# Performance work log

Measured on AMD Instinct MI355X. Metric: run time of the kernel, lower is better.

## Reference

```python
import jax, jax.numpy as jnp
import numpy as np

N_NODES = 524288
N_EDGES = 2097152
N_GRAPHS = 16384
COMP_DIM = 3539
PROT_DIM = 384
GNN_HID = 64
G_EMB = 128
HID = 256


def setup_inputs() -> dict:
    key = jax.random.key(0)
    ks = jax.random.split(key, 16)
    def lin(k, fan_in, fan_out):
        b = 1.0 / np.sqrt(fan_in)
        kw, kb = jax.random.split(k)
        return (jax.random.uniform(kw, (fan_in, fan_out), jnp.float32, -b, b),
                jax.random.uniform(kb, (fan_out,), jnp.float32, -b, b))
    W1, b1 = lin(ks[0], 1, GNN_HID)
    W2, b2 = lin(ks[1], GNN_HID, GNN_HID)
    Wg, bg = lin(ks[2], GNN_HID, G_EMB)
    Wf1, bf1 = lin(ks[3], G_EMB + COMP_DIM + PROT_DIM, HID)
    Wf2, bf2 = lin(ks[4], HID, 1)
    node_x = jax.random.normal(ks[5], (N_NODES, 1), jnp.float32)
    compound_feat = jax.random.normal(ks[6], (N_GRAPHS, COMP_DIM), jnp.float32)
    protein_feat = jax.random.normal(ks[7], (N_GRAPHS, PROT_DIM), jnp.float32)
    edge_index = jax.random.randint(ks[8], (2, N_EDGES), 0, N_NODES, jnp.int64 if jax.config.jax_enable_x64 else jnp.int32)
    batch = jnp.sort(jax.random.randint(ks[9], (N_NODES,), 0, N_GRAPHS, jnp.int32))
    return {"node_x": node_x, "compound_feat": compound_feat, "protein_feat": protein_feat,
            "edge_index": edge_index, "batch": batch,
            "W1": W1, "b1": b1, "W2": W2, "b2": b2, "Wg": Wg, "bg": bg,
            "Wf1": Wf1, "bf1": bf1, "Wf2": Wf2, "bf2": bf2}


def _gcn_norm(edge_index, num_nodes):
    # add self-loops, then symmetric normalization (PyG GCNConv default)
    loop = jnp.arange(num_nodes, dtype=edge_index.dtype)
    row = jnp.concatenate([edge_index[0], loop])
    col = jnp.concatenate([edge_index[1], loop])
    deg = jax.ops.segment_sum(jnp.ones_like(col, jnp.float32), col, num_segments=num_nodes)
    dinv = jnp.where(deg > 0, jax.lax.rsqrt(deg), 0.0)
    norm = dinv[row] * dinv[col]
    return row, col, norm


def _gcn_conv(x, W, b, row, col, norm, num_nodes):
    h = x @ W  # [N, out]
    out = jax.ops.segment_sum(norm[:, None] * h[row], col, num_segments=num_nodes)
    return out + b


def reference(node_x, compound_feat, protein_feat, edge_index, batch,
              W1, b1, W2, b2, Wg, bg, Wf1, bf1, Wf2, bf2):
    N = node_x.shape[0]
    B = compound_feat.shape[0]
    row, col, norm = _gcn_norm(edge_index, N)
    x = jax.nn.relu(_gcn_conv(node_x, W1, b1, row, col, norm, N))
    x = jax.nn.relu(_gcn_conv(x, W2, b2, row, col, norm, N))
    # global mean pool per graph
    sums = jax.ops.segment_sum(x, batch, num_segments=B)
    cnts = jax.ops.segment_sum(jnp.ones((N,), jnp.float32), batch, num_segments=B)
    pooled = sums / jnp.maximum(cnts, 1.0)[:, None]
    g = pooled @ Wg + bg  # [B, G_EMB]
    combined = jnp.concatenate([g, compound_feat, protein_feat], axis=1)
    h = jax.nn.relu(combined @ Wf1 + bf1)
    return jax.nn.sigmoid(h @ Wf2 + bf2)
```

## Files before the change

### kernel.cpp

```cpp
#include <hip/hip_runtime.h>

#define NN 524288
#define NE 2097152
#define NG 16384
#define CDIM 3539
#define PDIM 384
#define GH 64
#define GE 128
#define HIDD 256
#define KD (GE + CDIM + PDIM)
#define KP 4096

typedef short bf16x8 __attribute__((ext_vector_type(8)));
typedef unsigned short u16x8 __attribute__((ext_vector_type(8)));
typedef float f32x4 __attribute__((ext_vector_type(4)));

__device__ inline unsigned short f2bf(float f) {
    unsigned int u = __float_as_uint(f);
    u += 0x7FFF + ((u >> 16) & 1);
    return (unsigned short)(u >> 16);
}

__global__ void k_init(int* __restrict__ idg, float* __restrict__ sums) {
    int i = blockIdx.x * blockDim.x + threadIdx.x;
    if (i < NN) idg[i] = 0;
    if (i < NG * GH) sums[i] = 0.0f;
}

__global__ void k_deg(const int* __restrict__ ei, int* __restrict__ idg,
                      int* __restrict__ eseq) {
    int e = blockIdx.x * blockDim.x + threadIdx.x;
    eseq[e] = atomicAdd(&idg[ei[NE + e]], 1);
}

__global__ void k_prep(const float* __restrict__ node_x, const int* __restrict__ idg,
                       float2* __restrict__ f2a, int* __restrict__ ecnt) {
    int n = blockIdx.x * blockDim.x + threadIdx.x;
    int c = idg[n];
    float di = rsqrtf((float)(c + 1));
    f2a[n] = make_float2(di * node_x[n], di);
    ecnt[n] = c;
}

__global__ void k_cnt(const int* __restrict__ batch, float* __restrict__ cnt) {
    int g = blockIdx.x * 256 + threadIdx.x;
    int lo = 0, hi = NN;
    while (lo < hi) { int mid = (lo + hi) >> 1; if (batch[mid] < g) lo = mid + 1; else hi = mid; }
    int lo2 = lo, hi2 = NN;
    while (lo2 < hi2) { int mid = (lo2 + hi2) >> 1; if (batch[mid] < g + 1) lo2 = mid + 1; else hi2 = mid; }
    cnt[g] = (float)(lo2 - lo);
}

__global__ void k_scan1(const int* __restrict__ ecnt, int* __restrict__ bsum) {
    __shared__ int ls[256];
    int t = threadIdx.x;
    ls[t] = ecnt[blockIdx.x * 256 + t];
    __syncthreads();
    for (int d = 128; d > 0; d >>= 1) { if (t < d) ls[t] += ls[t + d]; __syncthreads(); }
    if (t == 0) bsum[blockIdx.x] = ls[0];
}

__global__ void k_scan2(int* __restrict__ bsum) {
    __shared__ int ls[256];
    int t = threadIdx.x;
    int loc[8]; int s = 0;
#pragma unroll
    for (int i = 0; i < 8; i++) { loc[i] = bsum[t * 8 + i]; s += loc[i]; }
    ls[t] = s; __syncthreads();
    for (int d = 1; d < 256; d <<= 1) {
        int add = (t >= d) ? ls[t - d] : 0; __syncthreads();
        ls[t] += add; __syncthreads();
    }
    int run = ls[t] - s;
#pragma unroll
    for (int i = 0; i < 8; i++) { int tmp = loc[i]; bsum[t * 8 + i] = run; run += tmp; }
}

__global__ void k_scan3(const int* __restrict__ ecnt, const int* __restrict__ bsum,
                        int* __restrict__ offs) {
    __shared__ int ls[256];
    int t = threadIdx.x, n = blockIdx.x * 256 + t;
    int v = ecnt[n];
    ls[t] = v; __syncthreads();
    for (int d = 1; d < 256; d <<= 1) {
        int add = (t >= d) ? ls[t - d] : 0; __syncthreads();
        ls[t] += add; __syncthreads();
    }
    offs[n] = bsum[blockIdx.x] + ls[t] - v;
    if (n == 0) offs[NN] = NE;
}

__global__ void k_fill(const int* __restrict__ ei, const int* __restrict__ offs,
                       const int* __restrict__ eseq, int* __restrict__ csr) {
    int e = blockIdx.x * 256 + threadIdx.x;
    int r = ei[e], c = ei[NE + e];
    csr[offs[c] + eseq[e]] = r;
}

__global__ void k_sg(const int* __restrict__ offs, const int* __restrict__ csr,
                     const float2* __restrict__ f2a, float2* __restrict__ sd) {
    int n = blockIdx.x * 256 + threadIdx.x;
    int a = offs[n], b = offs[n + 1];
    float2 me = f2a[n];
    float sum = me.x;
    for (int e = a; e < b; e += 4) {
#pragma unroll
        for (int i = 0; i < 4; i++) {
            int ee = e + i;
            int r = csr[min(ee, b - 1)];
            float v = f2a[r].x;
            sum += (ee < b) ? v : 0.0f;
        }
    }
    sd[n] = make_float2(me.y * sum, me.y);
}

__global__ __launch_bounds__(256) void k_gx2(
        const int* __restrict__ offs, const int* __restrict__ csr,
        const float2* __restrict__ sd, const float* __restrict__ W1,
        const float* __restrict__ b1, const unsigned short* __restrict__ W2T,
        const float* __restrict__ b2, const int* __restrict__ batch,
        float* __restrict__ sums) {
    __shared__ unsigned short aggs[64][72];
    __shared__ float x2s[64][73];
    __shared__ int bloc[64];
    int t = threadIdx.x;
    int wv = t >> 6, lane = t & 63;
    int n0 = blockIdx.x * 64;
    int nw = n0 + wv * 16;
    if (t < 64) bloc[t] = batch[n0 + t];
    float w1j = W1[lane], b1j = b1[lane];
    int nl = nw + (lane & 15);
    int aL = offs[nl], bndL = offs[nl + 1];
    float2 sdL = sd[nl];

    int base   = __shfl(aL, 0, 64);
    int endAll = __shfl(bndL, 15, 64);

#define LOADB(dst, bs) do { int en = (bs) + lane;                        \
    dst = make_float2(0.0f, 0.0f);                                       \
    if (en < endAll) dst = sd[csr[en]]; } while (0)

    int bstart = base;
    float2 vcur, vnxt;
    LOADB(vcur, bstart);
    LOADB(vnxt, bstart + 64);

    for (int i = 0; i < 16; i++) {
        int a    = __shfl(aL, i, 64);
        int bnd  = __shfl(bndL, i, 64);
        float sx = __shfl(sdL.x, i, 64);
        float sy = __shfl(sdL.y, i, 64);
        float acc = sy * fmaxf(fmaf(sx, w1j, b1j), 0.0f);
        for (int e = a; e < bnd; ++e) {
            int slot = e - bstart;
            if (slot >= 64) {
                bstart += 64;
                slot -= 64;
                vcur = vnxt;
                LOADB(vnxt, bstart + 64);
            }
            float vx = __shfl(vcur.x, slot, 64);
            float vy = __shfl(vcur.y, slot, 64);
            acc = fmaf(vy, fmaxf(fmaf(vx, w1j, b1j), 0.0f), acc);
        }
        aggs[wv * 16 + i][lane] = f2bf(sy * acc);
    }
#undef LOADB

    __syncthreads();
    int lg = lane >> 4, lr = lane & 15;
    bf16x8 a0 = *reinterpret_cast<const bf16x8*>(&aggs[wv * 16 + lr][lg * 8]);
    bf16x8 a1 = *reinterpret_cast<const bf16x8*>(&aggs[wv * 16 + lr][32 + lg * 8]);
    f32x4 acc4[4];
#pragma unroll
    for (int jt = 0; jt < 4; jt++) acc4[jt] = (f32x4){0.f, 0.f, 0.f, 0.f};
#pragma unroll
    for (int jt = 0; jt < 4; jt++) {
        bf16x8 b0 = *reinterpret_cast<const bf16x8*>(W2T + (jt * 16 + lr) * GH + lg * 8);
        bf16x8 b1v = *reinterpret_cast<const bf16x8*>(W2T + (jt * 16 + lr) * GH + 32 + lg * 8);
        acc4[jt] = __builtin_amdgcn_mfma_f32_16x16x32_bf16(a0, b0, acc4[jt], 0, 0, 0);
        acc4[jt] = __builtin_amdgcn_mfma_f32_16x16x32_bf16(a1, b1v, acc4[jt], 0, 0, 0);
    }
#pragma unroll
    for (int jt = 0; jt < 4; jt++) {
        float bj = b2[jt * 16 + lr];
#pragma unroll
        for (int r = 0; r < 4; r++)
            x2s[wv * 16 + lg * 4 + r][jt * 16 + lr] = fmaxf(acc4[jt][r] + bj, 0.0f);
    }
    __syncthreads();
    for (int i = wv; i < 64; i += 4) {
        bool isStart = (i == 0) || (bloc[i] != bloc[i - 1]);
        if (isStart) {
            int g = bloc[i];
            float s = 0.0f;
            int k = i;
            do { s += x2s[k][lane]; k++; } while (k < 64 && bloc[k] == g);
            atomicAdd(&sums[g * GH + lane], s);
        }
    }
}

__global__ void k_graph(const float* __restrict__ sums, const float* __restrict__ cnt,
                        const float* __restrict__ Wg, const float* __restrict__ bg,
                        float* __restrict__ gemb) {
    __shared__ float wgs[GH * GE];
    __shared__ float ps[4 * GH];
    int t = threadIdx.x;
    for (int i = t; i < GH * GE; i += 256) wgs[i] = Wg[i];
    int gid = blockIdx.x * 256 + t;
    int g = gid >> 6, j = t & 63, w = t >> 6;
    float c = fmaxf(cnt[g], 1.0f);
    ps[t] = sums[g * GH + j] / c;
    __syncthreads();
    float o0 = bg[j], o1 = bg[GH + j];
#pragma unroll
    for (int k = 0; k < GH; k++) {
        float p = ps[w * GH + k];
        o0 = fmaf(p, wgs[k * GE + j], o0);
        o1 = fmaf(p, wgs[k * GE + GH + j], o1);
    }
    gemb[g * GE + j] = o0;
    gemb[g * GE + GH + j] = o1;
}

__global__ void k_wt(const float* __restrict__ Wf1, unsigned short* __restrict__ WT,
                     const float* __restrict__ W2, unsigned short* __restrict__ W2T) {
    if (blockIdx.x == 1024) {
        int t = threadIdx.x;
        for (int i = 0; i < 16; i++) {
            int idx = t * 16 + i;
            int j = idx >> 6, k = idx & 63;
            W2T[j * GH + k] = f2bf(W2[k * GH + j]);
        }
        return;
    }
    __shared__ float tl[32][33];
    int bk = blockIdx.x & 127;
    int bn = blockIdx.x >> 7;
    int tx = threadIdx.x & 31, ty = threadIdx.x >> 5;
    int k0 = bk * 32, n0 = bn * 32;
#pragma unroll
    for (int i = 0; i < 4; i++) {
        int k = k0 + ty + i * 8;
        tl[ty + i * 8][tx] = (k < KD) ? Wf1[k * HIDD + n0 + tx] : 0.0f;
    }
    __syncthreads();
#pragma unroll
    for (int i = 0; i < 4; i++) {
        int n = n0 + ty + i * 8;
        WT[n * KP + k0 + tx] = f2bf(tl[tx][ty + i * 8]);
    }
}

__global__ void k_comb(const float* __restrict__ gemb, const float* __restrict__ comp,
                       const float* __restrict__ prot, unsigned short* __restrict__ comb) {
    int idx = blockIdx.x * 256 + threadIdx.x;
    int g = idx >> 9;
    int k0 = (idx & 511) * 8;
    u16x8 r;
    if (k0 >= GE && k0 + 8 <= GE + CDIM) {
        float v[8];
        __builtin_memcpy(v, comp + (size_t)g * CDIM + (k0 - GE), 32);
#pragma unroll
        for (int i = 0; i < 8; i++) r[i] = f2bf(v[i]);
    } else {
#pragma unroll
        for (int i = 0; i < 8; i++) {
            int k = k0 + i;
            float v = 0.0f;
            if (k < GE) v = gemb[g * GE + k];
            else if (k < GE + CDIM) v = comp[(size_t)g * CDIM + (k - GE)];
            else if (k < KD) v = prot[g * PDIM + (k - GE - CDIM)];
            r[i] = f2bf(v);
        }
    }
    *reinterpret_cast<u16x8*>(comb + (size_t)idx * 8) = r;
}

typedef const __attribute__((address_space(1))) void gas_void;
typedef __attribute__((address_space(3))) void las_void;

__global__ __launch_bounds__(256) void k_gemm_mfma(
        const unsigned short* __restrict__ WT, const unsigned short* __restrict__ comb,
        const float* __restrict__ bf1, const float* __restrict__ Wf2,
        const float* __restrict__ bf2, float* __restrict__ out) {
    __shared__ unsigned short ldsA[2][256 * 32];
    __shared__ unsigned short ldsB[2][32 * 32];
    __shared__ float red[32];
    int t = threadIdx.x;
    int wv = t >> 6, lane = t & 63;
    int lg = lane >> 4, lr = lane & 15;
    int g0 = blockIdx.x * 32;
    int nbase = wv * 64;

    int rowp = lane >> 2;
    int kp = (lane & 3) * 8;

    if (t < 32) red[t] = 0.0f;

    f32x4 acc[4][2];
#pragma unroll
    for (int i = 0; i < 4; i++)
#pragma unroll
        for (int j = 0; j < 2; j++) acc[i][j] = (f32x4){0.f, 0.f, 0.f, 0.f};

#define STAGE(buf, k0) do {                                                                  \
    _Pragma("unroll")                                                                        \
    for (int i = 0; i < 4; i++)                                                              \
        __builtin_amdgcn_global_load_lds(                                                    \
            (gas_void*)(WT + (size_t)(wv * 64 + i * 16 + rowp) * KP + (k0) + kp),            \
            (las_void*)(&ldsA[buf][(wv * 64 + i * 16) * 32]), 16, 0, 0);                     \
    if (wv < 2)                                                                              \
        __builtin_amdgcn_global_load_lds(                                                    \
            (gas_void*)(comb + (size_t)(g0 + wv * 16 + rowp) * KP + (k0) + kp),              \
            (las_void*)(&ldsB[buf][(wv * 16) * 32]), 16, 0, 0);                              \
} while (0)

    STAGE(0, 0);
    __syncthreads();
#pragma unroll 1
    for (int s = 0; s < 128; ++s) {
        int cur = s & 1;
        if (s < 127) STAGE(cur ^ 1, (s + 1) * 32);
        bf16x8 a[4], b[2];
#pragma unroll
        for (int nt = 0; nt < 4; nt++)
            a[nt] = *reinterpret_cast<const bf16x8*>(&ldsA[cur][(nbase + nt * 16 + lr) * 32 + lg * 8]);
#pragma unroll
        for (int gt = 0; gt < 2; gt++)
            b[gt] = *reinterpret_cast<const bf16x8*>(&ldsB[cur][(gt * 16 + lr) * 32 + lg * 8]);
#pragma unroll
        for (int nt = 0; nt < 4; nt++)
#pragma unroll
            for (int gt = 0; gt < 2; gt++)
                acc[nt][gt] = __builtin_amdgcn_mfma_f32_16x16x32_bf16(a[nt], b[gt], acc[nt][gt], 0, 0, 0);
        __syncthreads();
    }
#undef STAGE

    float bf2c = bf2[0];
#pragma unroll
    for (int gt = 0; gt < 2; gt++) {
        float pv = 0.0f;
#pragma unroll
        for (int nt = 0; nt < 4; nt++) {
            int nb = nbase + nt * 16 + lg * 4;
#pragma unroll
            for (int r = 0; r < 4; r++) {
                float h = fmaxf(acc[nt][gt][r] + bf1[nb + r], 0.0f);
                pv = fmaf(h, Wf2[nb + r], pv);
            }
        }
        pv += __shfl_xor(pv, 16);
        pv += __shfl_xor(pv, 32);
        if (lane < 16) atomicAdd(&red[gt * 16 + lane], pv);
    }
    __syncthreads();
    if (t < 32) out[g0 + t] = 1.0f / (1.0f + expf(-(red[t] + bf2c)));
}

extern "C" void kernel_launch(void* const* d_in, const int* in_sizes, int n_in,
                              void* d_out, int out_size, void* d_ws, size_t ws_size,
                              hipStream_t stream) {
    const float* node_x = (const float*)d_in[0];
    const float* comp   = (const float*)d_in[1];
    const float* prot   = (const float*)d_in[2];
    const int*   ei     = (const int*)d_in[3];
    const int*   batch  = (const int*)d_in[4];
    const float* W1  = (const float*)d_in[5];
    const float* b1  = (const float*)d_in[6];
    const float* W2  = (const float*)d_in[7];
    const float* b2  = (const float*)d_in[8];
    const float* Wg  = (const float*)d_in[9];
    const float* bg  = (const float*)d_in[10];
    const float* Wf1 = (const float*)d_in[11];
    const float* bf1 = (const float*)d_in[12];
    const float* Wf2 = (const float*)d_in[13];
    const float* bf2 = (const float*)d_in[14];
    float* out = (float*)d_out;

    char* W = (char*)d_ws;
    unsigned short* comb = (unsigned short*)W;
    int*    idg     = (int*)(W + 0);
    float2* f2a     = (float2*)(W + 2097152);
    float2* sd      = (float2*)(W + 6291456);
    int*    ecnt    = (int*)(W + 10485760);
    int*    offs    = (int*)(W + 12582912);
    int*    bsum    = (int*)(W + 16777728);
    int*    csr     = (int*)(W + 16786432);
    float*  sums    = (float*)(W + 25175040);
    float*  cnt     = (float*)(W + 29369344);
    int*    eseq    = (int*)(W + 33554432);
    float*  gemb    = (float*)(W + 134217728);
    unsigned short* WT  = (unsigned short*)(W + 142606336);
    unsigned short* W2T = (unsigned short*)(W + 144703488);

    k_init<<<4096, 256, 0, stream>>>(idg, sums);
    k_wt<<<1025, 256, 0, stream>>>(Wf1, WT, W2, W2T);
    k_deg<<<NE / 256, 256, 0, stream>>>(ei, idg, eseq);
    k_prep<<<NN / 256, 256, 0, stream>>>(node_x, idg, f2a, ecnt);
    k_cnt<<<NG / 256, 256, 0, stream>>>(batch, cnt);
    k_scan1<<<NN / 256, 256, 0, stream>>>(ecnt, bsum);
    k_scan2<<<1, 256, 0, stream>>>(bsum);
    k_scan3<<<NN / 256, 256, 0, stream>>>(ecnt, bsum, offs);
    k_fill<<<NE / 256, 256, 0, stream>>>(ei, offs, eseq, csr);
    k_sg<<<NN / 256, 256, 0, stream>>>(offs, csr, f2a, sd);
    k_gx2<<<NN / 64, 256, 0, stream>>>(offs, csr, sd, W1, b1, W2T, b2, batch, sums);
    k_graph<<<NG * GH / 256, 256, 0, stream>>>(sums, cnt, Wg, bg, gemb);
    k_comb<<<NG * KP / (256 * 8), 256, 0, stream>>>(gemb, comp, prot, comb);
    k_gemm_mfma<<<NG / 32, 256, 0, stream>>>(WT, comb, bf1, Wf2, bf2, out);
}
```

Before: 499.4 us.

## Split GEMM K across two wave groups with larger graph tile and vectorize comb

The final GEMM now uses 512-thread blocks covering 64 graphs instead of 32. The waves are split into two K-halves, each accumulating 2048 of the K dimension, and the partial sums are combined through LDS before the epilogue. This halves the number of K iterations per wave and doubles reuse of the staged weight tile across more graphs, at the cost of more LDS, extra register accumulators and a reduction step. The comb kernel also gains vectorized paths for the gemb and protein segments and a zero-fill fast path for padding.

```diff
diff --git a/kernel.cpp b/kernel.cpp
--- a/kernel.cpp
+++ b/kernel.cpp
@@ -260,20 +260,31 @@
     int g = idx >> 9;
     int k0 = (idx & 511) * 8;
     u16x8 r;
-    if (k0 >= GE && k0 + 8 <= GE + CDIM) {
-        float v[8];
+    float v[8];
+    if (k0 + 8 <= GE) {
+        __builtin_memcpy(v, gemb + (size_t)g * GE + k0, 32);
+#pragma unroll
+        for (int i = 0; i < 8; i++) r[i] = f2bf(v[i]);
+    } else if (k0 >= GE && k0 + 8 <= GE + CDIM) {
         __builtin_memcpy(v, comp + (size_t)g * CDIM + (k0 - GE), 32);
 #pragma unroll
         for (int i = 0; i < 8; i++) r[i] = f2bf(v[i]);
+    } else if (k0 >= GE + CDIM && k0 + 8 <= KD) {
+        __builtin_memcpy(v, prot + (size_t)g * PDIM + (k0 - GE - CDIM), 32);
+#pragma unroll
+        for (int i = 0; i < 8; i++) r[i] = f2bf(v[i]);
+    } else if (k0 >= KD) {
+#pragma unroll
+        for (int i = 0; i < 8; i++) r[i] = 0;
     } else {
 #pragma unroll
         for (int i = 0; i < 8; i++) {
             int k = k0 + i;
-            float v = 0.0f;
-            if (k < GE) v = gemb[g * GE + k];
-            else if (k < GE + CDIM) v = comp[(size_t)g * CDIM + (k - GE)];
-            else if (k < KD) v = prot[g * PDIM + (k - GE - CDIM)];
-            r[i] = f2bf(v);
+            float x = 0.0f;
+            if (k < GE) x = gemb[g * GE + k];
+            else if (k < GE + CDIM) x = comp[(size_t)g * CDIM + (k - GE)];
+            else if (k < KD) x = prot[g * PDIM + (k - GE - CDIM)];
+            r[i] = f2bf(x);
         }
     }
     *reinterpret_cast<u16x8*>(comb + (size_t)idx * 8) = r;
@@ -282,83 +293,114 @@
 typedef const __attribute__((address_space(1))) void gas_void;
 typedef __attribute__((address_space(3))) void las_void;
 
-__global__ __launch_bounds__(256) void k_gemm_mfma(
+__global__ __launch_bounds__(512) void k_gemm_mfma(
         const unsigned short* __restrict__ WT, const unsigned short* __restrict__ comb,
         const float* __restrict__ bf1, const float* __restrict__ Wf2,
         const float* __restrict__ bf2, float* __restrict__ out) {
-    __shared__ unsigned short ldsA[2][256 * 32];
-    __shared__ unsigned short ldsB[2][32 * 32];
-    __shared__ float red[32];
+    __shared__ unsigned short ldsA[2][2][256 * 32];
+    __shared__ unsigned short ldsB[2][2][64 * 32];
+    __shared__ float red[64];
     int t = threadIdx.x;
-    int wv = t >> 6, lane = t & 63;
+    int wv8 = t >> 6, lane = t & 63;
     int lg = lane >> 4, lr = lane & 15;
-    int g0 = blockIdx.x * 32;
-    int nbase = wv * 64;
+    int kh = wv8 >> 2;
+    int nwv = wv8 & 3;
+    int kbase = kh * 2048;
+    int g0 = blockIdx.x * 64;
+    int nbase = nwv * 64;
 
     int rowp = lane >> 2;
     int kp = (lane & 3) * 8;
 
-    if (t < 32) red[t] = 0.0f;
-
-    f32x4 acc[4][2];
+    if (t < 64) red[t] = 0.0f;
+
+    f32x4 acc[4][4];
 #pragma unroll
     for (int i = 0; i < 4; i++)
 #pragma unroll
-        for (int j = 0; j < 2; j++) acc[i][j] = (f32x4){0.f, 0.f, 0.f, 0.f};
+        for (int j = 0; j < 4; j++) acc[i][j] = (f32x4){0.f, 0.f, 0.f, 0.f};
 
 #define STAGE(buf, k0) do {                                                                  \
     _Pragma("unroll")                                                                        \
     for (int i = 0; i < 4; i++)                                                              \
         __builtin_amdgcn_global_load_lds(                                                    \
-            (gas_void*)(WT + (size_t)(wv * 64 + i * 16 + rowp) * KP + (k0) + kp),            \
-            (las_void*)(&ldsA[buf][(wv * 64 + i * 16) * 32]), 16, 0, 0);                     \
-    if (wv < 2)                                                                              \
-        __builtin_amdgcn_global_load_lds(                                                    \
-            (gas_void*)(comb + (size_t)(g0 + wv * 16 + rowp) * KP + (k0) + kp),              \
-            (las_void*)(&ldsB[buf][(wv * 16) * 32]), 16, 0, 0);                              \
+            (gas_void*)(WT + (size_t)(nwv * 64 + i * 16 + rowp) * KP + kbase + (k0) + kp),   \
+            (las_void*)(&ldsA[kh][buf][(nwv * 64 + i * 16) * 32]), 16, 0, 0);                \
+    __builtin_amdgcn_global_load_lds(                                                        \
+        (gas_void*)(comb + (size_t)(g0 + nwv * 16 + rowp) * KP + kbase + (k0) + kp),         \
+        (las_void*)(&ldsB[kh][buf][(nwv * 16) * 32]), 16, 0, 0);                             \
 } while (0)
 
     STAGE(0, 0);
     __syncthreads();
 #pragma unroll 1
-    for (int s = 0; s < 128; ++s) {
+    for (int s = 0; s < 64; ++s) {
         int cur = s & 1;
-        if (s < 127) STAGE(cur ^ 1, (s + 1) * 32);
-        bf16x8 a[4], b[2];
+        if (s < 63) STAGE(cur ^ 1, (s + 1) * 32);
+        bf16x8 a[4], b[4];
 #pragma unroll
         for (int nt = 0; nt < 4; nt++)
-            a[nt] = *reinterpret_cast<const bf16x8*>(&ldsA[cur][(nbase + nt * 16 + lr) * 32 + lg * 8]);
-#pragma unroll
-        for (int gt = 0; gt < 2; gt++)
-            b[gt] = *reinterpret_cast<const bf16x8*>(&ldsB[cur][(gt * 16 + lr) * 32 + lg * 8]);
+            a[nt] = *reinterpret_cast<const bf16x8*>(&ldsA[kh][cur][(nbase + nt * 16 + lr) * 32 + lg * 8]);
+#pragma unroll
+        for (int gt = 0; gt < 4; gt++)
+            b[gt] = *reinterpret_cast<const bf16x8*>(&ldsB[kh][cur][(gt * 16 + lr) * 32 + lg * 8]);
 #pragma unroll
         for (int nt = 0; nt < 4; nt++)
 #pragma unroll
-            for (int gt = 0; gt < 2; gt++)
+            for (int gt = 0; gt < 4; gt++)
                 acc[nt][gt] = __builtin_amdgcn_mfma_f32_16x16x32_bf16(a[nt], b[gt], acc[nt][gt], 0, 0, 0);
         __syncthreads();
     }
 #undef STAGE
 
+    float* cbuf = (float*)&ldsA[0][0][0];
+#pragma unroll
+    for (int round = 0; round < 2; ++round) {
+        if (kh == 1 && (nwv >> 1) == round) {
+            int slot = nwv & 1;
+#pragma unroll
+            for (int nt = 0; nt < 4; nt++)
+#pragma unroll
+                for (int gt = 0; gt < 4; gt++)
+#pragma unroll
+                    for (int r = 0; r < 4; r++)
+                        cbuf[slot * 4160 + lane * 65 + nt * 16 + gt * 4 + r] = acc[nt][gt][r];
+        }
+        __syncthreads();
+        if (kh == 0 && (nwv >> 1) == round) {
+            int slot = nwv & 1;
+#pragma unroll
+            for (int nt = 0; nt < 4; nt++)
+#pragma unroll
+                for (int gt = 0; gt < 4; gt++)
+#pragma unroll
+                    for (int r = 0; r < 4; r++)
+                        acc[nt][gt][r] += cbuf[slot * 4160 + lane * 65 + nt * 16 + gt * 4 + r];
+        }
+        __syncthreads();
+    }
+
     float bf2c = bf2[0];
-#pragma unroll
-    for (int gt = 0; gt < 2; gt++) {
-        float pv = 0.0f;
-#pragma unroll
-        for (int nt = 0; nt < 4; nt++) {
-            int nb = nbase + nt * 16 + lg * 4;
-#pragma unroll
-            for (int r = 0; r < 4; r++) {
-                float h = fmaxf(acc[nt][gt][r] + bf1[nb + r], 0.0f);
-                pv = fmaf(h, Wf2[nb + r], pv);
+    if (kh == 0) {
+#pragma unroll
+        for (int gt = 0; gt < 4; gt++) {
+            float pv = 0.0f;
+#pragma unroll
+            for (int nt = 0; nt < 4; nt++) {
+                int nb = nbase + nt * 16 + lg * 4;
+#pragma unroll
+                for (int r = 0; r < 4; r++) {
+                    float h = fmaxf(acc[nt][gt][r] + bf1[nb + r], 0.0f);
+                    pv = fmaf(h, Wf2[nb + r], pv);
+                }
             }
-        }
-        pv += __shfl_xor(pv, 16);
-        pv += __shfl_xor(pv, 32);
-        if (lane < 16) atomicAdd(&red[gt * 16 + lane], pv);
-    }
-    __syncthreads();
-    if (t < 32) out[g0 + t] = 1.0f / (1.0f + expf(-(red[t] + bf2c)));
+            pv += __shfl_xor(pv, 16);
+            pv += __shfl_xor(pv, 32);
+            if (lane < 16) atomicAdd(&red[gt * 16 + lane], pv);
+        }
+    }
+    __syncthreads();
+    if (t < 64) out[g0 + t] = 1.0f / (1.0f + expf(-(red[t] + bf2c)));
 }
 
 extern "C" void kernel_launch(void* const* d_in, const int* in_sizes, int n_in,
@@ -410,5 +452,5 @@
     k_gx2<<<NN / 64, 256, 0, stream>>>(offs, csr, sd, W1, b1, W2T, b2, batch, sums);
     k_graph<<<NG * GH / 256, 256, 0, stream>>>(sums, cnt, Wg, bg, gemb);
     k_comb<<<NG * KP / (256 * 8), 256, 0, stream>>>(gemb, comp, prot, comb);
-    k_gemm_mfma<<<NG / 32, 256, 0, stream>>>(WT, comb, bf1, Wf2, bf2, out);
-}
+    k_gemm_mfma<<<NG / 64, 512, 0, stream>>>(WT, comb, bf1, Wf2, bf2, out);
+}
```

Measured after the change: 494.3 us. No clear change (-1.0%).
